# Kernel tuning notes

Hardware: AMD Instinct MI355X
Metric: run time of the kernel (lower is better)

## Reference

```python
import jax, jax.numpy as jnp
import numpy as np

N_NODES = 50000
N_EDGES = 800000
D = 64  # node_dim == edge_dim
NEG_SLOPE = 0.2
EPS = 1e-5


def _lin_params(key, d_in, d_out):
    k1, k2 = jax.random.split(key)
    bound = 1.0 / np.sqrt(d_in)
    W = jax.random.uniform(k1, (d_out, d_in), minval=-bound, maxval=bound, dtype=jnp.float32)
    b = jax.random.uniform(k2, (d_out,), minval=-bound, maxval=bound, dtype=jnp.float32)
    return W, b


def setup_inputs() -> dict:
    key = jax.random.key(0)
    ks = jax.random.split(key, 12)
    V = jax.random.normal(ks[0], (N_NODES, D), dtype=jnp.float32)
    E = jax.random.normal(ks[1], (N_EDGES, D), dtype=jnp.float32)
    src = jax.random.randint(ks[2], (N_EDGES,), 0, N_NODES, dtype=jnp.int32)
    dst = jax.random.randint(ks[3], (N_EDGES,), 0, N_NODES, dtype=jnp.int32)
    pA_w, pA_b = _lin_params(ks[4], D, D)   # NodePooling.A
    pB_w, pB_b = _lin_params(ks[5], D, D)   # NodePooling.B
    mW1, mb1 = _lin_params(ks[6], D, D)     # edge MLP layer 1
    mW2, mb2 = _lin_params(ks[7], D, D)     # edge MLP layer 2
    BW, Bb = _lin_params(ks[8], D, D)       # GenMessage.B (scale)
    CW, Cb = _lin_params(ks[9], D, D)       # GenMessage.C (shift)
    return {"V": V, "E": E, "src": src, "dst": dst,
            "pA_w": pA_w, "pA_b": pA_b, "pB_w": pB_w, "pB_b": pB_b,
            "mW1": mW1, "mb1": mb1, "mW2": mW2, "mb2": mb2,
            "BW": BW, "Bb": Bb, "CW": CW, "Cb": Cb}


def _lrelu(x):
    return jnp.where(x >= 0, x, NEG_SLOPE * x)


def reference(V, E, src, dst, pA_w, pA_b, pB_w, pB_b, mW1, mb1, mW2, mb2, BW, Bb, CW, Cb):
    n = V.shape[0]
    # V = act(V); NodePooling: B(lrelu(A(V)))
    Va = _lrelu(V)
    Vp = _lrelu(Va @ pA_w.T + pA_b) @ pB_w.T + pB_b  # [N, D]
    # edge MLP on edge features (2 Linear+ReLU layers)
    x = jax.nn.relu(E @ mW1.T + mb1)
    x = jax.nn.relu(x @ mW2.T + mb2)                  # [E, D]
    scale = jax.nn.sigmoid(x @ BW.T + Bb)
    shift = x @ CW.T + Cb
    # gathered src features, gated affine message
    M1 = scale * Vp[src] + shift                      # [E, D]
    M2 = M1 * M1
    # segment-mean onto dst (DGL fn.mean); zero for isolated nodes
    deg = jax.ops.segment_sum(jnp.ones((dst.shape[0],), jnp.float32), dst, num_segments=n)
    denom = jnp.maximum(deg, 1.0)[:, None]
    V1 = jax.ops.segment_sum(M1, dst, num_segments=n) / denom
    V2 = jax.ops.segment_sum(M2, dst, num_segments=n) / denom
    return jnp.sqrt(jax.nn.relu(V2 - V1) + EPS)
```

## Files before the change

kernel.cpp:

```cpp
#include <hip/hip_runtime.h>

#define NN 50000
#define NE 800000
#define DDIM 64
#define PADX 68
#define PADK 72
#define NB_SCAN ((NN + 255) / 256)
#define NEG_SLOPE 0.2f
#define EPS_V 1e-5f

typedef short bf16x8 __attribute__((ext_vector_type(8)));
typedef float f32x4 __attribute__((ext_vector_type(4)));

__device__ __forceinline__ float lrelu_f(float x) { return x >= 0.0f ? x : NEG_SLOPE * x; }

__device__ __forceinline__ unsigned short bf16_rn(float x) {
    union { float f; unsigned int u; } c; c.f = x;
    unsigned int r = c.u + 0x7FFF + ((c.u >> 16) & 1);
    return (unsigned short)(r >> 16);
}
__device__ __forceinline__ float bf16_tof(unsigned short h) {
    union { float f; unsigned int u; } c; c.u = ((unsigned int)h) << 16;
    return c.f;
}

__device__ __forceinline__ void mma_tile(float acc[16], const float* __restrict__ XT,
                                         const float* __restrict__ Wc, int e0, int f0)
{
    #pragma unroll 4
    for (int kk = 0; kk < DDIM; kk += 4) {
        float4 A0 = *(const float4*)&XT[(kk+0)*PADX + e0];
        float4 A1 = *(const float4*)&XT[(kk+1)*PADX + e0];
        float4 A2 = *(const float4*)&XT[(kk+2)*PADX + e0];
        float4 A3 = *(const float4*)&XT[(kk+3)*PADX + e0];
        float4 B0 = *(const float4*)&Wc[(f0+0)*PADX + kk];
        float4 B1 = *(const float4*)&Wc[(f0+1)*PADX + kk];
        float4 B2 = *(const float4*)&Wc[(f0+2)*PADX + kk];
        float4 B3 = *(const float4*)&Wc[(f0+3)*PADX + kk];
        const float a[4][4] = {{A0.x,A0.y,A0.z,A0.w},{A1.x,A1.y,A1.z,A1.w},
                               {A2.x,A2.y,A2.z,A2.w},{A3.x,A3.y,A3.z,A3.w}};
        const float b[4][4] = {{B0.x,B0.y,B0.z,B0.w},{B1.x,B1.y,B1.z,B1.w},
                               {B2.x,B2.y,B2.z,B2.w},{B3.x,B3.y,B3.z,B3.w}};
        #pragma unroll
        for (int j = 0; j < 4; ++j)
            #pragma unroll
            for (int i = 0; i < 4; ++i)
                #pragma unroll
                for (int q = 0; q < 4; ++q)
                    acc[i*4+j] = fmaf(a[q][i], b[j][q], acc[i*4+j]);
    }
}

__device__ __forceinline__ void load_w_f32(float* __restrict__ Wc, const float* __restrict__ Wg, int tid)
{
    #pragma unroll
    for (int c = 0; c < 4; ++c) {
        int idx = (c << 10) + (tid << 2);
        int f = idx >> 6, k = idx & 63;
        *(float4*)&Wc[f*PADX + k] = *(const float4*)&Wg[idx];
    }
}

__global__ __launch_bounds__(256, 3)
void node_pool_kernel(const float* __restrict__ V,
                      const float* __restrict__ Aw, const float* __restrict__ Ab,
                      const float* __restrict__ Bw, const float* __restrict__ Bbv,
                      float* __restrict__ Vp)
{
    __shared__ float Wc[DDIM*PADX];
    __shared__ float XT[DDIM*PADX];
    const int tid = threadIdx.x;
    const int nb = blockIdx.x * 64;
    const int e0 = (tid & 15) << 2;
    const int f0 = (tid >> 4) << 2;

    #pragma unroll
    for (int c = 0; c < 4; ++c) {
        int idx = (c << 10) + (tid << 2);
        int e = idx >> 6, d = idx & 63;
        int row = nb + e; if (row > NN-1) row = NN-1;
        float4 v = *(const float4*)&V[(size_t)row*DDIM + d];
        XT[(d+0)*PADX + e] = lrelu_f(v.x);
        XT[(d+1)*PADX + e] = lrelu_f(v.y);
        XT[(d+2)*PADX + e] = lrelu_f(v.z);
        XT[(d+3)*PADX + e] = lrelu_f(v.w);
    }
    load_w_f32(Wc, Aw, tid);
    __syncthreads();

    float acc[16];
    #pragma unroll
    for (int i = 0; i < 16; ++i) acc[i] = 0.f;
    mma_tile(acc, XT, Wc, e0, f0);
    __syncthreads();

    {
        float4 bv = *(const float4*)&Ab[f0];
        const float ba[4] = {bv.x, bv.y, bv.z, bv.w};
        #pragma unroll
        for (int j = 0; j < 4; ++j) {
            float4 v;
            v.x = lrelu_f(acc[0*4+j] + ba[j]);
            v.y = lrelu_f(acc[1*4+j] + ba[j]);
            v.z = lrelu_f(acc[2*4+j] + ba[j]);
            v.w = lrelu_f(acc[3*4+j] + ba[j]);
            *(float4*)&XT[(f0+j)*PADX + e0] = v;
        }
    }
    load_w_f32(Wc, Bw, tid);
    __syncthreads();

    float acc2[16];
    #pragma unroll
    for (int i = 0; i < 16; ++i) acc2[i] = 0.f;
    mma_tile(acc2, XT, Wc, e0, f0);

    float4 bv = *(const float4*)&Bbv[f0];
    #pragma unroll
    for (int i = 0; i < 4; ++i) {
        int row = nb + e0 + i;
        if (row < NN) {
            float4 o;
            o.x = acc2[i*4+0] + bv.x;
            o.y = acc2[i*4+1] + bv.y;
            o.z = acc2[i*4+2] + bv.z;
            o.w = acc2[i*4+3] + bv.w;
            *(float4*)&Vp[(size_t)row*DDIM + f0] = o;
        }
    }
}

__global__ __launch_bounds__(256)
void hist_kernel(const int* __restrict__ dst, int* __restrict__ degi)
{
    int e = blockIdx.x * 256 + threadIdx.x;
    if (e < NE) atomicAdd(&degi[dst[e]], 1);
}

__global__ __launch_bounds__(256)
void scan1_kernel(const int* __restrict__ degi, int* __restrict__ linc, int* __restrict__ bsum)
{
    __shared__ int ws[4];
    const int tid = threadIdx.x;
    const int lane = tid & 63, wv = tid >> 6;
    int i = blockIdx.x * 256 + tid;
    int v = (i < NN) ? degi[i] : 0;
    int sc = v;
    #pragma unroll
    for (int off = 1; off < 64; off <<= 1) {
        int t = __shfl_up(sc, off, 64);
        if (lane >= off) sc += t;
    }
    if (lane == 63) ws[wv] = sc;
    __syncthreads();
    int wb = 0;
    #pragma unroll
    for (int w = 0; w < 4; ++w) if (w < wv) wb += ws[w];
    int incl = sc + wb;
    if (i < NN) linc[i] = incl;
    if (tid == 255) bsum[blockIdx.x] = incl;
}

__global__ __launch_bounds__(256)
void scan2_kernel(const int* __restrict__ bsum, int* __restrict__ bbase)
{
    __shared__ int ws[4];
    const int tid = threadIdx.x;
    const int lane = tid & 63, wv = tid >> 6;
    int v = (tid < NB_SCAN) ? bsum[tid] : 0;
    int sc = v;
    #pragma unroll
    for (int off = 1; off < 64; off <<= 1) {
        int t = __shfl_up(sc, off, 64);
        if (lane >= off) sc += t;
    }
    if (lane == 63) ws[wv] = sc;
    __syncthreads();
    int wb = 0;
    #pragma unroll
    for (int w = 0; w < 4; ++w) if (w < wv) wb += ws[w];
    if (tid < NB_SCAN) bbase[tid] = sc + wb - v;
}

__global__ __launch_bounds__(256)
void scan3_kernel(const int* __restrict__ degi, const int* __restrict__ linc,
                  const int* __restrict__ bbase, int* __restrict__ curs)
{
    int i = blockIdx.x * 256 + threadIdx.x;
    if (i < NN) curs[i] = bbase[blockIdx.x] + linc[i] - degi[i];
}

__global__ __launch_bounds__(256)
void scatter_kernel(const int* __restrict__ dst, int* __restrict__ cursor, int* __restrict__ eidx)
{
    int e = blockIdx.x * 256 + threadIdx.x;
    if (e < NE) {
        int p = atomicAdd(&cursor[dst[e]], 1);
        eidx[p] = e;
    }
}

__device__ __forceinline__ void stage_w(short* __restrict__ Wh, short* __restrict__ Wl,
                                        const float* __restrict__ Wg, int tid)
{
    #pragma unroll
    for (int c = 0; c < 4; ++c) {
        int idx = (c << 10) + (tid << 2);
        int f = idx >> 6, k = idx & 63;
        float4 v = *(const float4*)&Wg[idx];
        ushort4 h, l;
        h.x = bf16_rn(v.x); l.x = bf16_rn(v.x - bf16_tof(h.x));
        h.y = bf16_rn(v.y); l.y = bf16_rn(v.y - bf16_tof(h.y));
        h.z = bf16_rn(v.z); l.z = bf16_rn(v.z - bf16_tof(h.z));
        h.w = bf16_rn(v.w); l.w = bf16_rn(v.w - bf16_tof(h.w));
        *(ushort4*)&Wh[f*PADK + k] = h;
        *(ushort4*)&Wl[f*PADK + k] = l;
    }
}

__device__ __forceinline__ void mfma_gemm(const short* __restrict__ Xh, const short* __restrict__ Xl,
                                          const short* __restrict__ Wh, const short* __restrict__ Wl,
                                          int wv, int lane, f32x4 acc[4])
{
    const int m = lane & 15, kg = lane >> 4;
    const int arow = (wv*16 + m)*PADK + kg*8;
    #pragma unroll
    for (int ks = 0; ks < 2; ++ks) {
        bf16x8 ah = *(const bf16x8*)&Xh[arow + ks*32];
        bf16x8 al = *(const bf16x8*)&Xl[arow + ks*32];
        #pragma unroll
        for (int t = 0; t < 4; ++t) {
            int boff = (t*16 + m)*PADK + kg*8 + ks*32;
            bf16x8 bh = *(const bf16x8*)&Wh[boff];
            bf16x8 bl = *(const bf16x8*)&Wl[boff];
            acc[t] = __builtin_amdgcn_mfma_f32_16x16x32_bf16(al, bh, acc[t], 0, 0, 0);
            acc[t] = __builtin_amdgcn_mfma_f32_16x16x32_bf16(ah, bl, acc[t], 0, 0, 0);
            acc[t] = __builtin_amdgcn_mfma_f32_16x16x32_bf16(ah, bh, acc[t], 0, 0, 0);
        }
    }
}

__device__ __forceinline__ void repack_relu(short* __restrict__ Xh, short* __restrict__ Xl,
                                            const f32x4 acc[4], const float* __restrict__ bias,
                                            int wv, int lane)
{
    const int n = lane & 15, mg = lane >> 4;
    #pragma unroll
    for (int t = 0; t < 4; ++t) {
        float b = bias[t*16 + n];
        #pragma unroll
        for (int r = 0; r < 4; ++r) {
            float y = fmaxf(acc[t][r] + b, 0.0f);
            int e = wv*16 + mg*4 + r;
            unsigned short h = bf16_rn(y);
            float lof = y - bf16_tof(h);
            Xh[e*PADK + t*16 + n] = (short)h;
            Xl[e*PADK + t*16 + n] = (short)bf16_rn(lof);
        }
    }
}

__global__ __launch_bounds__(256, 4)
void edge_kernel(const float* __restrict__ Eg,
                 const int* __restrict__ src, const int* __restrict__ dst,
                 const int* __restrict__ eidx,
                 const float* __restrict__ W1, const float* __restrict__ b1,
                 const float* __restrict__ W2, const float* __restrict__ b2,
                 const float* __restrict__ WB, const float* __restrict__ bB,
                 const float* __restrict__ WC, const float* __restrict__ bC,
                 const float* __restrict__ Vp,
                 float* __restrict__ S1, float* __restrict__ S2)
{
    __shared__ __align__(16) char smem[4 * 64 * PADK * 2];
    __shared__ int srcs[64], dsts[64];
    short* Xh = (short*)smem;
    short* Xl = Xh + 64*PADK;
    short* Wh = Xl + 64*PADK;
    short* Wl = Wh + 64*PADK;
    float* M1T = (float*)smem;
    float* M2T = M1T + 64*PADX;

    const int tid = threadIdx.x;
    const int lane = tid & 63, wv = tid >> 6;
    const int eb = blockIdx.x * 64;

    #pragma unroll
    for (int c = 0; c < 4; ++c) {
        int idx = (c << 10) + (tid << 2);
        int e = idx >> 6, d = idx & 63;
        int eg = eidx[eb + e];
        float4 v = *(const float4*)&Eg[(size_t)eg*DDIM + d];
        ushort4 h, l;
        h.x = bf16_rn(v.x); l.x = bf16_rn(v.x - bf16_tof(h.x));
        h.y = bf16_rn(v.y); l.y = bf16_rn(v.y - bf16_tof(h.y));
        h.z = bf16_rn(v.z); l.z = bf16_rn(v.z - bf16_tof(h.z));
        h.w = bf16_rn(v.w); l.w = bf16_rn(v.w - bf16_tof(h.w));
        *(ushort4*)&Xh[e*PADK + d] = h;
        *(ushort4*)&Xl[e*PADK + d] = l;
    }
    if (tid < 64) {
        int eg = eidx[eb + tid];
        srcs[tid] = src[eg];
        dsts[tid] = dst[eg];
    }
    stage_w(Wh, Wl, W1, tid);
    __syncthreads();

    f32x4 acc[4];
    #pragma unroll
    for (int t = 0; t < 4; ++t) acc[t] = (f32x4){0.f, 0.f, 0.f, 0.f};
    mfma_gemm(Xh, Xl, Wh, Wl, wv, lane, acc);
    __syncthreads();
    repack_relu(Xh, Xl, acc, b1, wv, lane);
    stage_w(Wh, Wl, W2, tid);
    __syncthreads();

    #pragma unroll
    for (int t = 0; t < 4; ++t) acc[t] = (f32x4){0.f, 0.f, 0.f, 0.f};
    mfma_gemm(Xh, Xl, Wh, Wl, wv, lane, acc);
    __syncthreads();
    repack_relu(Xh, Xl, acc, b2, wv, lane);
    stage_w(Wh, Wl, WB, tid);
    __syncthreads();

    f32x4 accS[4];
    #pragma unroll
    for (int t = 0; t < 4; ++t) accS[t] = (f32x4){0.f, 0.f, 0.f, 0.f};
    mfma_gemm(Xh, Xl, Wh, Wl, wv, lane, accS);
    __syncthreads();
    stage_w(Wh, Wl, WC, tid);
    __syncthreads();

    f32x4 accH[4];
    #pragma unroll
    for (int t = 0; t < 4; ++t) accH[t] = (f32x4){0.f, 0.f, 0.f, 0.f};
    mfma_gemm(Xh, Xl, Wh, Wl, wv, lane, accH);
    __syncthreads();

    {
        const int n = lane & 15, mg = lane >> 4;
        #pragma unroll
        for (int t = 0; t < 4; ++t)
            #pragma unroll
            for (int r = 0; r < 4; ++r) {
                int f = t*16 + n;
                int e = wv*16 + mg*4 + r;
                M1T[f*PADX + e] = accS[t][r];
                M2T[f*PADX + e] = accH[t][r];
            }
    }
    __syncthreads();

    const int e0 = (tid & 15) << 2;
    const int f0 = (tid >> 4) << 2;
    {
        float4 bBv = *(const float4*)&bB[f0];
        float4 bCv = *(const float4*)&bC[f0];
        const float bBa[4] = {bBv.x, bBv.y, bBv.z, bBv.w};
        const float bCa[4] = {bCv.x, bCv.y, bCv.z, bCv.w};
        #pragma unroll
        for (int i = 0; i < 4; ++i) {
            const int e  = e0 + i;
            const int sn = srcs[e];
            float4 vp = *(const float4*)&Vp[(size_t)sn*DDIM + f0];
            const float vpa[4] = {vp.x, vp.y, vp.z, vp.w};
            #pragma unroll
            for (int j = 0; j < 4; ++j) {
                float sPre = M1T[(f0+j)*PADX + e] + bBa[j];
                float hPre = M2T[(f0+j)*PADX + e] + bCa[j];
                float sg = 1.0f / (1.0f + __expf(-sPre));
                float m1 = sg * vpa[j] + hPre;
                M1T[(f0+j)*PADX + e] = m1;
                M2T[(f0+j)*PADX + e] = m1 * m1;
            }
        }
    }
    __syncthreads();

    const int f = tid >> 2;
    const int g = (tid & 3) << 4;
    float s1 = 0.f, s2 = 0.f;
    int prev = dsts[g];
    #pragma unroll 4
    for (int i = 0; i < 16; ++i) {
        int dn = dsts[g + i];
        float m1 = M1T[f*PADX + g + i];
        float m2 = M2T[f*PADX + g + i];
        if (dn != prev) {
            atomicAdd(&S1[(size_t)prev*DDIM + f], s1);
            atomicAdd(&S2[(size_t)prev*DDIM + f], s2);
            s1 = 0.f; s2 = 0.f; prev = dn;
        }
        s1 += m1; s2 += m2;
    }
    atomicAdd(&S1[(size_t)prev*DDIM + f], s1);
    atomicAdd(&S2[(size_t)prev*DDIM + f], s2);
}

__global__ __launch_bounds__(256)
void finalize_kernel(const float* __restrict__ S1, const float* __restrict__ S2,
                     const int* __restrict__ degi, float* __restrict__ out)
{
    int gid = blockIdx.x * blockDim.x + threadIdx.x;
    if (gid >= NN*DDIM) return;
    int n = gid >> 6;
    float dn = (float)degi[n];
    dn = dn > 1.0f ? dn : 1.0f;
    float v = (S2[gid] - S1[gid]) / dn;
    out[gid] = sqrtf(fmaxf(v, 0.0f) + EPS_V);
}

extern "C" void kernel_launch(void* const* d_in, const int* in_sizes, int n_in,
                              void* d_out, int out_size, void* d_ws, size_t ws_size,
                              hipStream_t stream) {
    const float* V   = (const float*)d_in[0];
    const float* Eg  = (const float*)d_in[1];
    const int*   src = (const int*)d_in[2];
    const int*   dst = (const int*)d_in[3];
    const float* pAw = (const float*)d_in[4];
    const float* pAb = (const float*)d_in[5];
    const float* pBw = (const float*)d_in[6];
    const float* pBb = (const float*)d_in[7];
    const float* mW1 = (const float*)d_in[8];
    const float* mb1 = (const float*)d_in[9];
    const float* mW2 = (const float*)d_in[10];
    const float* mb2 = (const float*)d_in[11];
    const float* BW  = (const float*)d_in[12];
    const float* Bb  = (const float*)d_in[13];
    const float* CW  = (const float*)d_in[14];
    const float* Cb  = (const float*)d_in[15];
    float* out = (float*)d_out;

    float* ws    = (float*)d_ws;
    float* Vp    = ws;
    float* S1    = ws + (size_t)NN*DDIM;
    float* S2    = ws + (size_t)2*NN*DDIM;
    int*   degi  = (int*)(ws + (size_t)3*NN*DDIM);
    int*   curs  = degi + NN;
    int*   linc  = curs + NN;
    int*   bsum  = linc + NN;
    int*   bbase = bsum + NB_SCAN;
    int*   eidx  = bbase + NB_SCAN;

    hipMemsetAsync(S1, 0, (size_t)(2*NN*DDIM + NN) * sizeof(float), stream);

    node_pool_kernel<<<(NN + 63)/64, 256, 0, stream>>>(V, pAw, pAb, pBw, pBb, Vp);
    hist_kernel<<<(NE + 255)/256, 256, 0, stream>>>(dst, degi);
    scan1_kernel<<<NB_SCAN, 256, 0, stream>>>(degi, linc, bsum);
    scan2_kernel<<<1, 256, 0, stream>>>(bsum, bbase);
    scan3_kernel<<<NB_SCAN, 256, 0, stream>>>(degi, linc, bbase, curs);
    scatter_kernel<<<(NE + 255)/256, 256, 0, stream>>>(dst, curs, eidx);
    edge_kernel<<<NE/64, 256, 0, stream>>>(Eg, src, dst, eidx, mW1, mb1, mW2, mb2,
                                           BW, Bb, CW, Cb, Vp, S1, S2);
    finalize_kernel<<<(NN*DDIM + 255)/256, 256, 0, stream>>>(S1, S2, degi, out);
}
```

Measured before the change: 598.0 us.

## Pre-pack MFMA weight fragments, fuse histogram and scan kernels, trim edge-kernel LDS

A new prep kernel splits the four edge-MLP weight matrices once into bf16 hi/lo MFMA fragment layout in global memory. The edge kernel then loads those fragments straight into registers instead of restaging and converting each weight matrix in shared memory per block, so its LDS footprint and barriers shrink. The degree histogram is folded into node_pool_kernel as a grid-stride loop, and scan2/scan3 merge into one kernel, cutting launches. The gating epilogue now runs directly on MFMA accumulators, stores only M1 in LDS with a new padding, and forms M2 by squaring at reduction time. The extra weight registers lower the occupancy hint from 4 to 3 blocks per CU.

```diff
diff --git a/kernel.cpp b/kernel.cpp
--- a/kernel.cpp
+++ b/kernel.cpp
@@ -5,6 +5,7 @@
 #define DDIM 64
 #define PADX 68
 #define PADK 72
+#define PADM 69
 #define NB_SCAN ((NN + 255) / 256)
 #define NEG_SLOPE 0.2f
 #define EPS_V 1e-5f
@@ -65,7 +66,8 @@
 void node_pool_kernel(const float* __restrict__ V,
                       const float* __restrict__ Aw, const float* __restrict__ Ab,
                       const float* __restrict__ Bw, const float* __restrict__ Bbv,
-                      float* __restrict__ Vp)
+                      float* __restrict__ Vp,
+                      const int* __restrict__ dst, int* __restrict__ degi)
 {
     __shared__ float Wc[DDIM*PADX];
     __shared__ float XT[DDIM*PADX];
@@ -128,13 +130,29 @@
             *(float4*)&Vp[(size_t)row*DDIM + f0] = o;
         }
     }
+
+    const int stride = gridDim.x * 256;
+    for (int e = blockIdx.x * 256 + tid; e < NE; e += stride)
+        atomicAdd(&degi[dst[e]], 1);
 }
 
 __global__ __launch_bounds__(256)
-void hist_kernel(const int* __restrict__ dst, int* __restrict__ degi)
-{
-    int e = blockIdx.x * 256 + threadIdx.x;
-    if (e < NE) atomicAdd(&degi[dst[e]], 1);
+void prep_w_kernel(const float* __restrict__ W1, const float* __restrict__ W2,
+                   const float* __restrict__ WB, const float* __restrict__ WC,
+                   short* __restrict__ WF)
+{
+    int gid = blockIdx.x * 256 + threadIdx.x;
+    int L = gid >> 12, r = gid & 4095;
+    int t = r >> 10, ks = (r >> 9) & 1, lane = (r >> 3) & 63, j = r & 7;
+    const float* Ws = (L == 0) ? W1 : (L == 1) ? W2 : (L == 2) ? WB : WC;
+    int n = lane & 15, kg = lane >> 4;
+    int f = t*16 + n, k = ks*32 + kg*8 + j;
+    float v = Ws[f*64 + k];
+    unsigned short h = bf16_rn(v);
+    unsigned short l = bf16_rn(v - bf16_tof(h));
+    int base = L*8192 + ((t*2 + ks)*2)*512 + lane*8 + j;
+    WF[base]       = (short)h;
+    WF[base + 512] = (short)l;
 }
 
 __global__ __launch_bounds__(256)
@@ -162,9 +180,11 @@
 }
 
 __global__ __launch_bounds__(256)
-void scan2_kernel(const int* __restrict__ bsum, int* __restrict__ bbase)
+void scan23_kernel(const int* __restrict__ degi, const int* __restrict__ linc,
+                   const int* __restrict__ bsum, int* __restrict__ curs)
 {
     __shared__ int ws[4];
+    __shared__ int base_s;
     const int tid = threadIdx.x;
     const int lane = tid & 63, wv = tid >> 6;
     int v = (tid < NB_SCAN) ? bsum[tid] : 0;
@@ -179,15 +199,10 @@
     int wb = 0;
     #pragma unroll
     for (int w = 0; w < 4; ++w) if (w < wv) wb += ws[w];
-    if (tid < NB_SCAN) bbase[tid] = sc + wb - v;
-}
-
-__global__ __launch_bounds__(256)
-void scan3_kernel(const int* __restrict__ degi, const int* __restrict__ linc,
-                  const int* __restrict__ bbase, int* __restrict__ curs)
-{
-    int i = blockIdx.x * 256 + threadIdx.x;
-    if (i < NN) curs[i] = bbase[blockIdx.x] + linc[i] - degi[i];
+    if (tid == blockIdx.x) base_s = sc + wb - v;
+    __syncthreads();
+    int i = blockIdx.x * 256 + tid;
+    if (i < NN) curs[i] = base_s + linc[i] - degi[i];
 }
 
 __global__ __launch_bounds__(256)
@@ -200,43 +215,36 @@
     }
 }
 
-__device__ __forceinline__ void stage_w(short* __restrict__ Wh, short* __restrict__ Wl,
-                                        const float* __restrict__ Wg, int tid)
-{
-    #pragma unroll
-    for (int c = 0; c < 4; ++c) {
-        int idx = (c << 10) + (tid << 2);
-        int f = idx >> 6, k = idx & 63;
-        float4 v = *(const float4*)&Wg[idx];
-        ushort4 h, l;
-        h.x = bf16_rn(v.x); l.x = bf16_rn(v.x - bf16_tof(h.x));
-        h.y = bf16_rn(v.y); l.y = bf16_rn(v.y - bf16_tof(h.y));
-        h.z = bf16_rn(v.z); l.z = bf16_rn(v.z - bf16_tof(h.z));
-        h.w = bf16_rn(v.w); l.w = bf16_rn(v.w - bf16_tof(h.w));
-        *(ushort4*)&Wh[f*PADK + k] = h;
-        *(ushort4*)&Wl[f*PADK + k] = l;
-    }
-}
-
-__device__ __forceinline__ void mfma_gemm(const short* __restrict__ Xh, const short* __restrict__ Xl,
-                                          const short* __restrict__ Wh, const short* __restrict__ Wl,
-                                          int wv, int lane, f32x4 acc[4])
+struct WFrags { bf16x8 bh[4][2]; bf16x8 bl[4][2]; };
+
+__device__ __forceinline__ void load_wfrags(const short* __restrict__ WL, int lane, WFrags& w)
+{
+    #pragma unroll
+    for (int t = 0; t < 4; ++t)
+        #pragma unroll
+        for (int ks = 0; ks < 2; ++ks) {
+            w.bh[t][ks] = *(const bf16x8*)&WL[(((t*2 + ks)*2 + 0)*64 + lane)*8];
+            w.bl[t][ks] = *(const bf16x8*)&WL[(((t*2 + ks)*2 + 1)*64 + lane)*8];
+        }
+}
+
+__device__ __forceinline__ void mfma_gemm_r(const short* __restrict__ Xh, const short* __restrict__ Xl,
+                                            const WFrags& w, int wv, int lane, f32x4 acc[4])
 {
     const int m = lane & 15, kg = lane >> 4;
     const int arow = (wv*16 + m)*PADK + kg*8;
-    #pragma unroll
-    for (int ks = 0; ks < 2; ++ks) {
-        bf16x8 ah = *(const bf16x8*)&Xh[arow + ks*32];
-        bf16x8 al = *(const bf16x8*)&Xl[arow + ks*32];
-        #pragma unroll
-        for (int t = 0; t < 4; ++t) {
-            int boff = (t*16 + m)*PADK + kg*8 + ks*32;
-            bf16x8 bh = *(const bf16x8*)&Wh[boff];
-            bf16x8 bl = *(const bf16x8*)&Wl[boff];
-            acc[t] = __builtin_amdgcn_mfma_f32_16x16x32_bf16(al, bh, acc[t], 0, 0, 0);
-            acc[t] = __builtin_amdgcn_mfma_f32_16x16x32_bf16(ah, bl, acc[t], 0, 0, 0);
-            acc[t] = __builtin_amdgcn_mfma_f32_16x16x32_bf16(ah, bh, acc[t], 0, 0, 0);
-        }
+    bf16x8 ah0 = *(const bf16x8*)&Xh[arow];
+    bf16x8 al0 = *(const bf16x8*)&Xl[arow];
+    bf16x8 ah1 = *(const bf16x8*)&Xh[arow + 32];
+    bf16x8 al1 = *(const bf16x8*)&Xl[arow + 32];
+    #pragma unroll
+    for (int t = 0; t < 4; ++t) {
+        acc[t] = __builtin_amdgcn_mfma_f32_16x16x32_bf16(al0, w.bh[t][0], acc[t], 0, 0, 0);
+        acc[t] = __builtin_amdgcn_mfma_f32_16x16x32_bf16(ah0, w.bl[t][0], acc[t], 0, 0, 0);
+        acc[t] = __builtin_amdgcn_mfma_f32_16x16x32_bf16(ah0, w.bh[t][0], acc[t], 0, 0, 0);
+        acc[t] = __builtin_amdgcn_mfma_f32_16x16x32_bf16(al1, w.bh[t][1], acc[t], 0, 0, 0);
+        acc[t] = __builtin_amdgcn_mfma_f32_16x16x32_bf16(ah1, w.bl[t][1], acc[t], 0, 0, 0);
+        acc[t] = __builtin_amdgcn_mfma_f32_16x16x32_bf16(ah1, w.bh[t][1], acc[t], 0, 0, 0);
     }
 }
 
@@ -260,25 +268,21 @@
     }
 }
 
-__global__ __launch_bounds__(256, 4)
+__global__ __launch_bounds__(256, 3)
 void edge_kernel(const float* __restrict__ Eg,
                  const int* __restrict__ src, const int* __restrict__ dst,
                  const int* __restrict__ eidx,
-                 const float* __restrict__ W1, const float* __restrict__ b1,
-                 const float* __restrict__ W2, const float* __restrict__ b2,
-                 const float* __restrict__ WB, const float* __restrict__ bB,
-                 const float* __restrict__ WC, const float* __restrict__ bC,
+                 const short* __restrict__ WF,
+                 const float* __restrict__ b1, const float* __restrict__ b2,
+                 const float* __restrict__ bB, const float* __restrict__ bC,
                  const float* __restrict__ Vp,
                  float* __restrict__ S1, float* __restrict__ S2)
 {
-    __shared__ __align__(16) char smem[4 * 64 * PADK * 2];
+    __shared__ __align__(16) char smem[2 * 64 * PADK * 2];
     __shared__ int srcs[64], dsts[64];
     short* Xh = (short*)smem;
     short* Xl = Xh + 64*PADK;
-    short* Wh = Xl + 64*PADK;
-    short* Wl = Wh + 64*PADK;
     float* M1T = (float*)smem;
-    float* M2T = M1T + 64*PADX;
 
     const int tid = threadIdx.x;
     const int lane = tid & 63, wv = tid >> 6;
@@ -303,75 +307,51 @@
         srcs[tid] = src[eg];
         dsts[tid] = dst[eg];
     }
-    stage_w(Wh, Wl, W1, tid);
+    WFrags w;
+    load_wfrags(WF, lane, w);
     __syncthreads();
 
     f32x4 acc[4];
     #pragma unroll
     for (int t = 0; t < 4; ++t) acc[t] = (f32x4){0.f, 0.f, 0.f, 0.f};
-    mfma_gemm(Xh, Xl, Wh, Wl, wv, lane, acc);
+    mfma_gemm_r(Xh, Xl, w, wv, lane, acc);
     __syncthreads();
     repack_relu(Xh, Xl, acc, b1, wv, lane);
-    stage_w(Wh, Wl, W2, tid);
+    load_wfrags(WF + 8192, lane, w);
     __syncthreads();
 
     #pragma unroll
     for (int t = 0; t < 4; ++t) acc[t] = (f32x4){0.f, 0.f, 0.f, 0.f};
-    mfma_gemm(Xh, Xl, Wh, Wl, wv, lane, acc);
+    mfma_gemm_r(Xh, Xl, w, wv, lane, acc);
     __syncthreads();
     repack_relu(Xh, Xl, acc, b2, wv, lane);
-    stage_w(Wh, Wl, WB, tid);
-    __syncthreads();
-
-    f32x4 accS[4];
-    #pragma unroll
-    for (int t = 0; t < 4; ++t) accS[t] = (f32x4){0.f, 0.f, 0.f, 0.f};
-    mfma_gemm(Xh, Xl, Wh, Wl, wv, lane, accS);
-    __syncthreads();
-    stage_w(Wh, Wl, WC, tid);
-    __syncthreads();
-
-    f32x4 accH[4];
-    #pragma unroll
-    for (int t = 0; t < 4; ++t) accH[t] = (f32x4){0.f, 0.f, 0.f, 0.f};
-    mfma_gemm(Xh, Xl, Wh, Wl, wv, lane, accH);
+    load_wfrags(WF + 2*8192, lane, w);
+    __syncthreads();
+
+    f32x4 accS[4], accH[4];
+    #pragma unroll
+    for (int t = 0; t < 4; ++t) { accS[t] = (f32x4){0.f,0.f,0.f,0.f}; accH[t] = (f32x4){0.f,0.f,0.f,0.f}; }
+    mfma_gemm_r(Xh, Xl, w, wv, lane, accS);
+    load_wfrags(WF + 3*8192, lane, w);
+    mfma_gemm_r(Xh, Xl, w, wv, lane, accH);
     __syncthreads();
 
     {
         const int n = lane & 15, mg = lane >> 4;
-        #pragma unroll
-        for (int t = 0; t < 4; ++t)
+        int sn[4];
+        #pragma unroll
+        for (int r = 0; r < 4; ++r) sn[r] = srcs[wv*16 + mg*4 + r];
+        #pragma unroll
+        for (int t = 0; t < 4; ++t) {
+            const int f = t*16 + n;
+            const float bBv = bB[f];
+            const float bCv = bC[f];
             #pragma unroll
             for (int r = 0; r < 4; ++r) {
-                int f = t*16 + n;
-                int e = wv*16 + mg*4 + r;
-                M1T[f*PADX + e] = accS[t][r];
-                M2T[f*PADX + e] = accH[t][r];
-            }
-    }
-    __syncthreads();
-
-    const int e0 = (tid & 15) << 2;
-    const int f0 = (tid >> 4) << 2;
-    {
-        float4 bBv = *(const float4*)&bB[f0];
-        float4 bCv = *(const float4*)&bC[f0];
-        const float bBa[4] = {bBv.x, bBv.y, bBv.z, bBv.w};
-        const float bCa[4] = {bCv.x, bCv.y, bCv.z, bCv.w};
-        #pragma unroll
-        for (int i = 0; i < 4; ++i) {
-            const int e  = e0 + i;
-            const int sn = srcs[e];
-            float4 vp = *(const float4*)&Vp[(size_t)sn*DDIM + f0];
-            const float vpa[4] = {vp.x, vp.y, vp.z, vp.w};
-            #pragma unroll
-            for (int j = 0; j < 4; ++j) {
-                float sPre = M1T[(f0+j)*PADX + e] + bBa[j];
-                float hPre = M2T[(f0+j)*PADX + e] + bCa[j];
-                float sg = 1.0f / (1.0f + __expf(-sPre));
-                float m1 = sg * vpa[j] + hPre;
-                M1T[(f0+j)*PADX + e] = m1;
-                M2T[(f0+j)*PADX + e] = m1 * m1;
+                float vp = Vp[(size_t)sn[r]*DDIM + f];
+                float sg = 1.0f / (1.0f + __expf(-(accS[t][r] + bBv)));
+                float m1 = fmaf(sg, vp, accH[t][r] + bCv);
+                M1T[f*PADM + wv*16 + mg*4 + r] = m1;
             }
         }
     }
@@ -384,8 +364,8 @@
     #pragma unroll 4
     for (int i = 0; i < 16; ++i) {
         int dn = dsts[g + i];
-        float m1 = M1T[f*PADX + g + i];
-        float m2 = M2T[f*PADX + g + i];
+        float m1 = M1T[f*PADM + g + i];
+        float m2 = m1 * m1;
         if (dn != prev) {
             atomicAdd(&S1[(size_t)prev*DDIM + f], s1);
             atomicAdd(&S2[(size_t)prev*DDIM + f], s2);
@@ -441,16 +421,16 @@
     int*   bsum  = linc + NN;
     int*   bbase = bsum + NB_SCAN;
     int*   eidx  = bbase + NB_SCAN;
+    short* WF    = (short*)(eidx + NE);
 
     hipMemsetAsync(S1, 0, (size_t)(2*NN*DDIM + NN) * sizeof(float), stream);
 
-    node_pool_kernel<<<(NN + 63)/64, 256, 0, stream>>>(V, pAw, pAb, pBw, pBb, Vp);
-    hist_kernel<<<(NE + 255)/256, 256, 0, stream>>>(dst, degi);
+    prep_w_kernel<<<64, 256, 0, stream>>>(mW1, mW2, BW, CW, WF);
+    node_pool_kernel<<<(NN + 63)/64, 256, 0, stream>>>(V, pAw, pAb, pBw, pBb, Vp, dst, degi);
     scan1_kernel<<<NB_SCAN, 256, 0, stream>>>(degi, linc, bsum);
-    scan2_kernel<<<1, 256, 0, stream>>>(bsum, bbase);
-    scan3_kernel<<<NB_SCAN, 256, 0, stream>>>(degi, linc, bbase, curs);
+    scan23_kernel<<<NB_SCAN, 256, 0, stream>>>(degi, linc, bsum, curs);
     scatter_kernel<<<(NE + 255)/256, 256, 0, stream>>>(dst, curs, eidx);
-    edge_kernel<<<NE/64, 256, 0, stream>>>(Eg, src, dst, eidx, mW1, mb1, mW2, mb2,
-                                           BW, Bb, CW, Cb, Vp, S1, S2);
+    edge_kernel<<<NE/64, 256, 0, stream>>>(Eg, src, dst, eidx, WF,
+                                           mb1, mb2, Bb, Cb, Vp, S1, S2);
     finalize_kernel<<<(NN*DDIM + 255)/256, 256, 0, stream>>>(S1, S2, degi, out);
 }
```

Measured after the change: 584.4 us. 2.3% less time.
